# Kernel tuning notes

Hardware: AMD Instinct MI355X
Metric: run time of the kernel (lower is better)

The kernel has to match this reference:

```python
import jax, jax.numpy as jnp
import numpy as np

BN_EPS = 1e-5


def _bn(x, gamma, beta):
    # BatchNorm1d in training mode: batch mean, biased variance
    m = jnp.mean(x, axis=0)
    v = jnp.var(x, axis=0)
    return (x - m) * jax.lax.rsqrt(v + BN_EPS) * gamma + beta


def _gin_rel(h_src, h_dst, src, dst, W1, W2, g1, b1, g2, b2):
    # GINConv (eps=0): sum-aggregate src features onto dst, add self feature
    n_dst = h_dst.shape[0]
    agg = jax.ops.segment_sum(h_src[src], dst, num_segments=n_dst)  # [N_dst, d]
    x = h_dst + agg
    # MLP: Linear -> BN -> ReLU -> Linear  (both Linears bias=False)
    h = jax.nn.relu(_bn(x @ W1, g1, b1)) @ W2
    # GINBase: BN -> ReLU
    return jax.nn.relu(_bn(h, g2, b2))


def setup_inputs() -> dict:
    key = jax.random.key(0)
    ks = jax.random.split(key, 12)
    N_U, N_I, E, D = 50000, 50000, 640000, 128
    s = 1.0 / np.sqrt(D)
    inp = {
        "h_user": jax.random.normal(ks[0], (N_U, D), jnp.float32),
        "h_item": jax.random.normal(ks[1], (N_I, D), jnp.float32),
        "src_rates": jax.random.randint(ks[2], (E,), 0, N_U, jnp.int32),
        "dst_rates": jax.random.randint(ks[3], (E,), 0, N_I, jnp.int32),
        "src_rev": jax.random.randint(ks[4], (E,), 0, N_I, jnp.int32),
        "dst_rev": jax.random.randint(ks[5], (E,), 0, N_U, jnp.int32),
        "W1_rates": jax.random.normal(ks[6], (D, D), jnp.float32) * s,
        "W2_rates": jax.random.normal(ks[7], (D, D), jnp.float32) * s,
        "g1_rates": jnp.ones((D,), jnp.float32),
        "b1_rates": jnp.zeros((D,), jnp.float32),
        "g2_rates": jnp.ones((D,), jnp.float32),
        "b2_rates": jnp.zeros((D,), jnp.float32),
        "W1_rev": jax.random.normal(ks[8], (D, D), jnp.float32) * s,
        "W2_rev": jax.random.normal(ks[9], (D, D), jnp.float32) * s,
        "g1_rev": jnp.ones((D,), jnp.float32),
        "b1_rev": jnp.zeros((D,), jnp.float32),
        "g2_rev": jnp.ones((D,), jnp.float32),
        "b2_rev": jnp.zeros((D,), jnp.float32),
    }
    return inp


def reference(h_user, h_item, src_rates, dst_rates, src_rev, dst_rev,
              W1_rates, W2_rates, g1_rates, b1_rates, g2_rates, b2_rates,
              W1_rev, W2_rev, g1_rev, b1_rev, g2_rev, b2_rev):
    # relation 'rates': user -> item; relation 'rated_by': item -> user
    out_item = _gin_rel(h_user, h_item, src_rates, dst_rates,
                        W1_rates, W2_rates, g1_rates, b1_rates, g2_rates, b2_rates)
    out_user = _gin_rel(h_item, h_user, src_rev, dst_rev,
                        W1_rev, W2_rev, g1_rev, b1_rev, g2_rev, b2_rev)
    # HeteroGraphConv sums per dst type; one relation per dst type here.
    # GINLayer squeezes each output (no-op for 2D tensors).
    return (out_user, out_item)
```

## Files before the change

kernel.cpp:

```cpp
#include <hip/hip_runtime.h>

#define D 128
#define NBUK 8
#define NCH 32
#define BWMAX 8192
#define FILL_FINE 2048
static constexpr float BN_EPS = 1e-5f;

typedef __attribute__((ext_vector_type(8))) short short8;
typedef __attribute__((ext_vector_type(4))) float f32x4;

__device__ __forceinline__ unsigned short f2bf(float f)
{
    unsigned u = __builtin_bit_cast(unsigned, f);
    unsigned r = u + 0x7fffu + ((u >> 16) & 1u);
    return (unsigned short)(r >> 16);
}
__device__ __forceinline__ float bflo(unsigned u)
{
    return __builtin_bit_cast(float, u << 16);
}
__device__ __forceinline__ float bfhi(unsigned u)
{
    return __builtin_bit_cast(float, u & 0xffff0000u);
}

struct CsrRel {
    const int* src; const int* dst;
    int* counts; int* offsets; int* bsum; int* perm; int* rank; int* pc;
    int E; int N; int nscan;
};
struct GatherRel {
    const unsigned short* hb; const float* hdst;
    const int* offsets; const int* perm;
    unsigned short* x; int N;
};
struct GemmRel {
    const unsigned short* X; const unsigned short* Wt;
    const float* insum; const float* insq; const float* gg; const float* bb;
    unsigned short* Y; float* osum; float* osq;
    int N; int ntiles;
};
struct OutRel {
    const unsigned short* z;
    const float* sum; const float* sq; const float* gg; const float* bb;
    float* out; int N;
};

__global__ __launch_bounds__(256) void prep_kernel(
    const float* __restrict__ hu, const float* __restrict__ hi,
    unsigned short* __restrict__ bu, unsigned short* __restrict__ bi8,
    int nu8, int ni8,
    const float* __restrict__ Wa, const float* __restrict__ Wb,
    const float* __restrict__ Wc, const float* __restrict__ Wd,
    unsigned short* __restrict__ wt, float* __restrict__ stats)
{
    const int t = threadIdx.x;
    if (blockIdx.x < 64) {
        const int wsel = blockIdx.x >> 4;
        const float* W = wsel == 0 ? Wa : wsel == 1 ? Wb : wsel == 2 ? Wc : Wd;
        unsigned short* out = wt + (size_t)wsel * D * D;
        const int tile = blockIdx.x & 15;
        const int k0 = (tile >> 2) * 32, n0 = (tile & 3) * 32;
        __shared__ float s[32][33];
        const int r = t >> 3, c = (t & 7) * 4;
        float4 v = *reinterpret_cast<const float4*>(W + (size_t)(k0 + r) * D + n0 + c);
        s[r][c] = v.x; s[r][c + 1] = v.y; s[r][c + 2] = v.z; s[r][c + 3] = v.w;
        __syncthreads();
        unsigned lo = (unsigned)f2bf(s[c][r]) | ((unsigned)f2bf(s[c + 1][r]) << 16);
        unsigned hi = (unsigned)f2bf(s[c + 2][r]) | ((unsigned)f2bf(s[c + 3][r]) << 16);
        *reinterpret_cast<uint2*>(out + (size_t)(n0 + r) * D + k0 + c) =
            make_uint2(lo, hi);
        return;
    }
    if (blockIdx.x == 64) {
        reinterpret_cast<float4*>(stats)[t] = make_float4(0.f, 0.f, 0.f, 0.f);
        return;
    }
    int i = (blockIdx.x - 65) * 256 + t;
    if (i >= nu8 + ni8) return;
    const float* s; unsigned short* d; int o;
    if (i < nu8) { s = hu; d = bu; o = i; }
    else         { s = hi; d = bi8; o = i - nu8; }
    float4 v0 = reinterpret_cast<const float4*>(s)[o * 2];
    float4 v1 = reinterpret_cast<const float4*>(s)[o * 2 + 1];
    uint4 r;
    r.x = (unsigned)f2bf(v0.x) | ((unsigned)f2bf(v0.y) << 16);
    r.y = (unsigned)f2bf(v0.z) | ((unsigned)f2bf(v0.w) << 16);
    r.z = (unsigned)f2bf(v1.x) | ((unsigned)f2bf(v1.y) << 16);
    r.w = (unsigned)f2bf(v1.z) | ((unsigned)f2bf(v1.w) << 16);
    reinterpret_cast<uint4*>(d)[o] = r;
}

__global__ __launch_bounds__(256) void hist_kernel(CsrRel r0, CsrRel r1)
{
    CsrRel r = blockIdx.y ? r1 : r0;
    __shared__ int h[BWMAX];
    const int b = blockIdx.x & (NBUK - 1);
    const int c = blockIdx.x >> 3;
    const int bw = (r.N + NBUK - 1) / NBUK;
    const int lo = b * bw;
    const int hi = min(lo + bw, r.N);
    const int CE = (r.E + NCH - 1) / NCH;
    const int e1 = min(c * CE + CE, r.E);

    for (int j = threadIdx.x; j < bw; j += 256) h[j] = 0;
    __syncthreads();
    for (int e = c * CE + threadIdx.x; e < e1; e += 256) {
        int d = r.dst[e];
        if (d >= lo && d < hi)
            r.rank[e] = atomicAdd(&h[d - lo], 1);
    }
    __syncthreads();
    int* out = r.pc + (size_t)(b * NCH + c) * bw;
    for (int j = threadIdx.x; j < bw; j += 256) out[j] = h[j];
}

__global__ __launch_bounds__(256) void chunkpfx_kernel(CsrRel r0, CsrRel r1)
{
    CsrRel r = blockIdx.y ? r1 : r0;
    const int t = threadIdx.x;
    int d = blockIdx.x * 256 + t;
    int s = 0;
    if (d < r.N) {
        const int bw = (r.N + NBUK - 1) / NBUK;
        int b = d / bw, j = d - b * bw;
        int* base = r.pc + (size_t)b * NCH * bw + j;
        for (int c = 0; c < NCH; ++c) {
            int v = base[(size_t)c * bw];
            base[(size_t)c * bw] = s;
            s += v;
        }
        r.counts[d] = s;
    }
    __shared__ int red[256];
    red[t] = s;
    __syncthreads();
    for (int off = 128; off > 0; off >>= 1) {
        if (t < off) red[t] += red[t + off];
        __syncthreads();
    }
    if (t == 0) r.bsum[blockIdx.x] = red[0];
}

__global__ __launch_bounds__(256) void scan_partials_kernel(CsrRel rr0, CsrRel rr1)
{
    CsrRel r = blockIdx.y ? rr1 : rr0;
    __shared__ int part[256];
    const int t = threadIdx.x;
    int v = (t < r.nscan) ? r.bsum[t] : 0;
    part[t] = v;
    __syncthreads();
    for (int off = 1; off < 256; off <<= 1) {
        int tmp = (t >= off) ? part[t - off] : 0;
        __syncthreads();
        part[t] += tmp;
        __syncthreads();
    }
    if (t < r.nscan) r.bsum[t] = part[t] - v;
}

__global__ __launch_bounds__(256) void scan_block_kernel(CsrRel rr0, CsrRel rr1)
{
    CsrRel r = blockIdx.y ? rr1 : rr0;
    if ((int)blockIdx.x >= r.nscan) return;
    __shared__ int part[256];
    const int t = threadIdx.x;
    const int d = blockIdx.x * 256 + t;
    int v = (d < r.N) ? r.counts[d] : 0;
    part[t] = v;
    __syncthreads();
    for (int off = 1; off < 256; off <<= 1) {
        int tmp = (t >= off) ? part[t - off] : 0;
        __syncthreads();
        part[t] += tmp;
        __syncthreads();
    }
    int excl = part[t] - v + r.bsum[blockIdx.x];
    if (d < r.N) {
        r.offsets[d] = excl;
        if (d == r.N - 1) r.offsets[r.N] = excl + v;
    }
}

__global__ __launch_bounds__(256) void fill_kernel(CsrRel rr0, CsrRel rr1)
{
    CsrRel r = blockIdx.y ? rr1 : rr0;
    const int b = blockIdx.x & (NBUK - 1);
    const int fc = blockIdx.x >> 3;
    const int f0 = fc * FILL_FINE;
    if (f0 >= r.E) return;
    const int f1 = min(f0 + FILL_FINE, r.E);
    const int bw = (r.N + NBUK - 1) / NBUK;
    const int lo = b * bw;
    const int hi = min(lo + bw, r.N);
    const int CE = (r.E + NCH - 1) / NCH;
    const int c0 = f0 / CE;
    const int cb = (c0 + 1) * CE;
    const int* pcb0 = r.pc + (size_t)(b * NCH + c0) * bw;
    const int* pcb1 = pcb0 + bw;
    for (int e = f0 + threadIdx.x; e < f1; e += 256) {
        int d = r.dst[e];
        if (d >= lo && d < hi) {
            const int* pcb = (e >= cb) ? pcb1 : pcb0;
            r.perm[r.offsets[d] + pcb[d - lo] + r.rank[e]] = r.src[e];
        }
    }
}

__global__ __launch_bounds__(256) void gather_agg_kernel(GatherRel g0, GatherRel g1)
{
    GatherRel g = blockIdx.y ? g1 : g0;
    int row = blockIdx.x * 4 + (threadIdx.x >> 6);
    row = __builtin_amdgcn_readfirstlane(row);
    if (row >= g.N) return;
    const int c = (threadIdx.x & 63) * 2;
    const int beg = g.offsets[row], end = g.offsets[row + 1];
    float2 acc = *reinterpret_cast<const float2*>(g.hdst + (size_t)row * D + c);
    const unsigned short* hb = g.hb;
    int i = beg;
    for (; i + 7 < end; i += 8) {
        unsigned u[8];
#pragma unroll
        for (int k = 0; k < 8; ++k) {
            int s = g.perm[i + k];
            u[k] = *reinterpret_cast<const unsigned*>(hb + (size_t)s * D + c);
        }
        float ax = 0.f, ay = 0.f;
#pragma unroll
        for (int k = 0; k < 8; ++k) { ax += bflo(u[k]); ay += bfhi(u[k]); }
        acc.x += ax;
        acc.y += ay;
    }
    if (i + 3 < end) {
        int s0 = g.perm[i], s1 = g.perm[i + 1];
        int s2 = g.perm[i + 2], s3 = g.perm[i + 3];
        unsigned u0 = *reinterpret_cast<const unsigned*>(hb + (size_t)s0 * D + c);
        unsigned u1 = *reinterpret_cast<const unsigned*>(hb + (size_t)s1 * D + c);
        unsigned u2 = *reinterpret_cast<const unsigned*>(hb + (size_t)s2 * D + c);
        unsigned u3 = *reinterpret_cast<const unsigned*>(hb + (size_t)s3 * D + c);
        acc.x += (bflo(u0) + bflo(u1)) + (bflo(u2) + bflo(u3));
        acc.y += (bfhi(u0) + bfhi(u1)) + (bfhi(u2) + bfhi(u3));
        i += 4;
    }
    for (; i < end; ++i) {
        unsigned u = *reinterpret_cast<const unsigned*>(hb + (size_t)g.perm[i] * D + c);
        acc.x += bflo(u);
        acc.y += bfhi(u);
    }
    unsigned o = (unsigned)f2bf(acc.x) | ((unsigned)f2bf(acc.y) << 16);
    *reinterpret_cast<unsigned*>(g.x + (size_t)row * D + c) = o;
}

__device__ __forceinline__ unsigned bnpack(unsigned u, float sLo, float sHi,
                                           float bLo, float bHi)
{
    float lo = fmaxf(fmaf(bflo(u), sLo, bLo), 0.f);
    float hi = fmaxf(fmaf(bfhi(u), sHi, bHi), 0.f);
    return (unsigned)f2bf(lo) | ((unsigned)f2bf(hi) << 16);
}

template <bool BN_IN>
__global__ __launch_bounds__(256, 2) void gemm_stats_kernel(GemmRel q0, GemmRel q1)
{
    GemmRel q = blockIdx.y ? q1 : q0;
    const int t = threadIdx.x;
    const int w = t >> 6;
    const int l = t & 63;
    const int lr = l & 15;
    const int lk = (l >> 4) << 3;

    __shared__ float s_sc[D], s_bi[D];
    if constexpr (BN_IN) {
        if (t < D) {
            float inv_n = 1.f / (float)q.N;
            float mean = q.insum[t] * inv_n;
            float var = fmaxf(q.insq[t] * inv_n - mean * mean, 0.f);
            float s = q.gg[t] * rsqrtf(var + BN_EPS);
            s_sc[t] = s;
            s_bi[t] = q.bb[t] - mean * s;
        }
        __syncthreads();
    }

    uint4 wf[4][8];
#pragma unroll
    for (int kk = 0; kk < 4; ++kk)
#pragma unroll
        for (int n = 0; n < 8; ++n)
            wf[kk][n] = *reinterpret_cast<const uint4*>(
                q.Wt + (size_t)(n * 16 + lr) * D + kk * 32 + lk);

    float ps[8], pq[8];
#pragma unroll
    for (int n = 0; n < 8; ++n) { ps[n] = 0.f; pq[n] = 0.f; }

    for (int tile = blockIdx.x; tile < q.ntiles; tile += gridDim.x) {
        const int arow = tile * 64 + w * 16 + lr;
        f32x4 acc[8];
#pragma unroll
        for (int n = 0; n < 8; ++n) acc[n] = (f32x4){0.f, 0.f, 0.f, 0.f};

#pragma unroll
        for (int kk = 0; kk < 4; ++kk) {
            uint4 a4 = make_uint4(0u, 0u, 0u, 0u);
            if (arow < q.N) {
                a4 = *reinterpret_cast<const uint4*>(
                    q.X + (size_t)arow * D + kk * 32 + lk);
                if constexpr (BN_IN) {
                    const int kb = kk * 32 + lk;
                    float4 s0 = *reinterpret_cast<const float4*>(&s_sc[kb]);
                    float4 s1 = *reinterpret_cast<const float4*>(&s_sc[kb + 4]);
                    float4 b0 = *reinterpret_cast<const float4*>(&s_bi[kb]);
                    float4 b1 = *reinterpret_cast<const float4*>(&s_bi[kb + 4]);
                    a4.x = bnpack(a4.x, s0.x, s0.y, b0.x, b0.y);
                    a4.y = bnpack(a4.y, s0.z, s0.w, b0.z, b0.w);
                    a4.z = bnpack(a4.z, s1.x, s1.y, b1.x, b1.y);
                    a4.w = bnpack(a4.w, s1.z, s1.w, b1.z, b1.w);
                }
            }
            short8 a = __builtin_bit_cast(short8, a4);
#pragma unroll
            for (int n = 0; n < 8; ++n)
                acc[n] = __builtin_amdgcn_mfma_f32_16x16x32_bf16(
                    a, __builtin_bit_cast(short8, wf[kk][n]), acc[n], 0, 0, 0);
        }

        const int orow = tile * 64 + w * 16 + (l >> 4) * 4;
#pragma unroll
        for (int n = 0; n < 8; ++n) {
#pragma unroll
            for (int j = 0; j < 4; ++j) {
                float v = acc[n][j];
                ps[n] += v;
                pq[n] += v * v;
                if (orow + j < q.N)
                    q.Y[(size_t)(orow + j) * D + n * 16 + lr] = f2bf(v);
            }
        }
    }

#pragma unroll
    for (int n = 0; n < 8; ++n) {
        ps[n] += __shfl_xor(ps[n], 16); ps[n] += __shfl_xor(ps[n], 32);
        pq[n] += __shfl_xor(pq[n], 16); pq[n] += __shfl_xor(pq[n], 32);
    }
    __shared__ float ssum[4][D], ssq[4][D];
    if (l < 16) {
#pragma unroll
        for (int n = 0; n < 8; ++n) {
            ssum[w][n * 16 + l] = ps[n];
            ssq[w][n * 16 + l]  = pq[n];
        }
    }
    __syncthreads();
    if (t < D) {
        float a = ssum[0][t] + ssum[1][t] + ssum[2][t] + ssum[3][t];
        float b = ssq[0][t] + ssq[1][t] + ssq[2][t] + ssq[3][t];
        atomicAdd(&q.osum[t], a);
        atomicAdd(&q.osq[t], b);
    }
}

__global__ __launch_bounds__(256) void bn_relu_out_kernel(OutRel o0, OutRel o1)
{
    OutRel o = blockIdx.y ? o1 : o0;
    __shared__ float s_sc[D], s_bi[D];
    if (threadIdx.x < D) {
        int c = threadIdx.x;
        float inv_n = 1.f / (float)o.N;
        float mean = o.sum[c] * inv_n;
        float var = fmaxf(o.sq[c] * inv_n - mean * mean, 0.f);
        float s = o.gg[c] * rsqrtf(var + BN_EPS);
        s_sc[c] = s;
        s_bi[c] = o.bb[c] - mean * s;
    }
    __syncthreads();

    const int n8 = o.N * (D / 8);
    for (int i = blockIdx.x * blockDim.x + threadIdx.x; i < n8;
         i += gridDim.x * blockDim.x) {
        uint4 z = reinterpret_cast<const uint4*>(o.z)[i];
        int c = (i * 8) & (D - 1);
        float4 s0 = *reinterpret_cast<const float4*>(&s_sc[c]);
        float4 s1 = *reinterpret_cast<const float4*>(&s_sc[c + 4]);
        float4 b0 = *reinterpret_cast<const float4*>(&s_bi[c]);
        float4 b1 = *reinterpret_cast<const float4*>(&s_bi[c + 4]);
        float4 r0, r1;
        r0.x = fmaxf(fmaf(bflo(z.x), s0.x, b0.x), 0.f);
        r0.y = fmaxf(fmaf(bfhi(z.x), s0.y, b0.y), 0.f);
        r0.z = fmaxf(fmaf(bflo(z.y), s0.z, b0.z), 0.f);
        r0.w = fmaxf(fmaf(bfhi(z.y), s0.w, b0.w), 0.f);
        r1.x = fmaxf(fmaf(bflo(z.z), s1.x, b1.x), 0.f);
        r1.y = fmaxf(fmaf(bfhi(z.z), s1.y, b1.y), 0.f);
        r1.z = fmaxf(fmaf(bflo(z.w), s1.z, b1.z), 0.f);
        r1.w = fmaxf(fmaf(bfhi(z.w), s1.w, b1.w), 0.f);
        reinterpret_cast<float4*>(o.out)[i * 2] = r0;
        reinterpret_cast<float4*>(o.out)[i * 2 + 1] = r1;
    }
}

extern "C" void kernel_launch(void* const* d_in, const int* in_sizes, int n_in,
                              void* d_out, int out_size, void* d_ws, size_t ws_size,
                              hipStream_t stream)
{
    const float* h_user   = (const float*)d_in[0];
    const float* h_item   = (const float*)d_in[1];
    const int* src_rates  = (const int*)d_in[2];
    const int* dst_rates  = (const int*)d_in[3];
    const int* src_rev    = (const int*)d_in[4];
    const int* dst_rev    = (const int*)d_in[5];
    const float* W1_rates = (const float*)d_in[6];
    const float* W2_rates = (const float*)d_in[7];
    const float* g1_rates = (const float*)d_in[8];
    const float* b1_rates = (const float*)d_in[9];
    const float* g2_rates = (const float*)d_in[10];
    const float* b2_rates = (const float*)d_in[11];
    const float* W1_rev   = (const float*)d_in[12];
    const float* W2_rev   = (const float*)d_in[13];
    const float* g1_rev   = (const float*)d_in[14];
    const float* b1_rev   = (const float*)d_in[15];
    const float* g2_rev   = (const float*)d_in[16];
    const float* b2_rev   = (const float*)d_in[17];

    const int n_user = in_sizes[0] / D;
    const int n_item = in_sizes[1] / D;
    const int E1 = in_sizes[2];
    const int E2 = in_sizes[4];

    const int bw0 = (n_item + NBUK - 1) / NBUK;
    const int bw1 = (n_user + NBUK - 1) / NBUK;

    char* p = (char*)d_ws;
    auto alloc = [&](size_t bytes) {
        char* q = p;
        p += (bytes + 255) & ~(size_t)255;
        return q;
    };
    unsigned short* hbu = (unsigned short*)alloc((size_t)n_user * D * 2);
    unsigned short* hbi = (unsigned short*)alloc((size_t)n_item * D * 2);
    unsigned short* xz0 = (unsigned short*)alloc((size_t)n_item * D * 2);
    unsigned short* xz1 = (unsigned short*)alloc((size_t)n_user * D * 2);
    unsigned short* yb0 = (unsigned short*)alloc((size_t)n_item * D * 2);
    unsigned short* yb1 = (unsigned short*)alloc((size_t)n_user * D * 2);
    unsigned short* wt  = (unsigned short*)alloc((size_t)4 * D * D * 2);
    float* stats   = (float*)alloc((size_t)8 * D * 4);
    int* counts0   = (int*)alloc((size_t)n_item * 4);
    int* counts1   = (int*)alloc((size_t)n_user * 4);
    int* offsets0  = (int*)alloc(((size_t)n_item + 1) * 4);
    int* offsets1  = (int*)alloc(((size_t)n_user + 1) * 4);
    int* bsum0     = (int*)alloc((size_t)256 * 4);
    int* bsum1     = (int*)alloc((size_t)256 * 4);
    int* perm0     = (int*)alloc((size_t)E1 * 4);
    int* perm1     = (int*)alloc((size_t)E2 * 4);
    int* rank0     = (int*)alloc((size_t)E1 * 4);
    int* rank1     = (int*)alloc((size_t)E2 * 4);
    int* pc0       = (int*)alloc((size_t)NBUK * NCH * bw0 * 4);
    int* pc1       = (int*)alloc((size_t)NBUK * NCH * bw1 * 4);

    float* out_user = (float*)d_out;
    float* out_item = out_user + (size_t)n_user * D;

    const int nu8 = n_user * D / 8, ni8 = n_item * D / 8;
    int pblocks = 65 + (nu8 + ni8 + 255) / 256;
    prep_kernel<<<pblocks, 256, 0, stream>>>(
        h_user, h_item, hbu, hbi, nu8, ni8,
        W1_rates, W2_rates, W1_rev, W2_rev, wt, stats);

    float* st0 = stats;
    float* st1 = stats + 4 * D;

    CsrRel c0 = {src_rates, dst_rates, counts0, offsets0, bsum0, perm0, rank0,
                 pc0, E1, n_item, (n_item + 255) / 256};
    CsrRel c1 = {src_rev, dst_rev, counts1, offsets1, bsum1, perm1, rank1,
                 pc1, E2, n_user, (n_user + 255) / 256};

    int ns = c0.nscan > c1.nscan ? c0.nscan : c1.nscan;
    int nmax = n_item > n_user ? n_item : n_user;
    int emax = E1 > E2 ? E1 : E2;
    hist_kernel<<<dim3(NBUK * NCH, 2), 256, 0, stream>>>(c0, c1);
    chunkpfx_kernel<<<dim3(ns, 2), 256, 0, stream>>>(c0, c1);
    scan_partials_kernel<<<dim3(1, 2), 256, 0, stream>>>(c0, c1);
    scan_block_kernel<<<dim3(ns, 2), 256, 0, stream>>>(c0, c1);
    int nfine = (emax + FILL_FINE - 1) / FILL_FINE;
    fill_kernel<<<dim3(NBUK * nfine, 2), 256, 0, stream>>>(c0, c1);

    GatherRel ga0 = {hbu, h_item, offsets0, perm0, xz0, n_item};
    GatherRel ga1 = {hbi, h_user, offsets1, perm1, xz1, n_user};
    int ab = (nmax + 3) / 4;
    gather_agg_kernel<<<dim3(ab, 2), 256, 0, stream>>>(ga0, ga1);

    const int nt0 = (n_item + 63) / 64, nt1 = (n_user + 63) / 64;
    int gx = nt0 > nt1 ? nt0 : nt1;
    if (gx > 256) gx = 256;

    GemmRel q10 = {xz0, wt,             nullptr, nullptr, nullptr, nullptr,
                   yb0, st0, st0 + D, n_item, nt0};
    GemmRel q11 = {xz1, wt + 2 * D * D, nullptr, nullptr, nullptr, nullptr,
                   yb1, st1, st1 + D, n_user, nt1};
    gemm_stats_kernel<false><<<dim3(gx, 2), 256, 0, stream>>>(q10, q11);

    GemmRel q20 = {yb0, wt + D * D,     st0, st0 + D, g1_rates, b1_rates,
                   xz0, st0 + 2 * D, st0 + 3 * D, n_item, nt0};
    GemmRel q21 = {yb1, wt + 3 * D * D, st1, st1 + D, g1_rev, b1_rev,
                   xz1, st1 + 2 * D, st1 + 3 * D, n_user, nt1};
    gemm_stats_kernel<true><<<dim3(gx, 2), 256, 0, stream>>>(q20, q21);

    OutRel o0 = {xz0, st0 + 2 * D, st0 + 3 * D, g2_rates, b2_rates,
                 out_item, n_item};
    OutRel o1 = {xz1, st1 + 2 * D, st1 + 3 * D, g2_rev, b2_rev,
                 out_user, n_user};
    int n8m = nmax * (D / 8);
    int ob = (n8m + 255) / 256;
    if (ob > 2048) ob = 2048;
    bn_relu_out_kernel<<<dim3(ob, 2), 256, 0, stream>>>(o0, o1);
}
```

Before: 206.3 us.

## Pack CSR histogram counters into 16-bit pairs to cover all destinations per block

```diff
diff --git a/kernel.cpp b/kernel.cpp
--- a/kernel.cpp
+++ b/kernel.cpp
@@ -2,9 +2,8 @@
 
 #define D 128
 #define NBUK 8
-#define NCH 32
-#define BWMAX 8192
-#define FILL_FINE 2048
+#define NCHF 128
+#define LDSW 32768
 static constexpr float BN_EPS = 1e-5f;
 
 typedef __attribute__((ext_vector_type(8))) short short8;
@@ -27,7 +26,8 @@
 
 struct CsrRel {
     const int* src; const int* dst;
-    int* counts; int* offsets; int* bsum; int* perm; int* rank; int* pc;
+    int* counts; int* offsets; int* bsum; int* perm;
+    unsigned short* rank16; unsigned* pc;
     int E; int N; int nscan;
 };
 struct GatherRel {
@@ -95,43 +95,61 @@
 __global__ __launch_bounds__(256) void hist_kernel(CsrRel r0, CsrRel r1)
 {
     CsrRel r = blockIdx.y ? r1 : r0;
-    __shared__ int h[BWMAX];
-    const int b = blockIdx.x & (NBUK - 1);
-    const int c = blockIdx.x >> 3;
-    const int bw = (r.N + NBUK - 1) / NBUK;
-    const int lo = b * bw;
-    const int hi = min(lo + bw, r.N);
-    const int CE = (r.E + NCH - 1) / NCH;
-    const int e1 = min(c * CE + CE, r.E);
-
-    for (int j = threadIdx.x; j < bw; j += 256) h[j] = 0;
-    __syncthreads();
-    for (int e = c * CE + threadIdx.x; e < e1; e += 256) {
+    __shared__ unsigned h2[LDSW];
+    const int t = threadIdx.x;
+    const int c = blockIdx.x;
+    const int CE = (r.E + NCHF - 1) / NCHF;
+    const int e0 = c * CE;
+    const int e1 = min(e0 + CE, r.E);
+    const int bw2 = (r.N + 1) >> 1;
+
+    const int bw4 = bw2 & ~3;
+    for (int i = t * 4; i < bw4; i += 1024)
+        *reinterpret_cast<uint4*>(&h2[i]) = make_uint4(0u, 0u, 0u, 0u);
+    for (int i = bw4 + t; i < bw2; i += 256) h2[i] = 0u;
+    __syncthreads();
+
+    for (int e = e0 + t; e < e1; e += 256) {
         int d = r.dst[e];
-        if (d >= lo && d < hi)
-            r.rank[e] = atomicAdd(&h[d - lo], 1);
-    }
-    __syncthreads();
-    int* out = r.pc + (size_t)(b * NCH + c) * bw;
-    for (int j = threadIdx.x; j < bw; j += 256) out[j] = h[j];
+        unsigned sh = (unsigned)(d & 1) * 16u;
+        unsigned old = atomicAdd(&h2[d >> 1], 1u << sh);
+        r.rank16[e] = (unsigned short)((old >> sh) & 0xffffu);
+    }
+    __syncthreads();
+
+    unsigned* out = r.pc + (size_t)c * bw2;
+    for (int i = t * 4; i < bw4; i += 1024)
+        *reinterpret_cast<uint4*>(&out[i]) = *reinterpret_cast<uint4*>(&h2[i]);
+    for (int i = bw4 + t; i < bw2; i += 256) out[i] = h2[i];
 }
 
 __global__ __launch_bounds__(256) void chunkpfx_kernel(CsrRel r0, CsrRel r1)
 {
     CsrRel r = blockIdx.y ? r1 : r0;
+    __shared__ unsigned lds[NCHF * 256];
     const int t = threadIdx.x;
-    int d = blockIdx.x * 256 + t;
+    const int j = blockIdx.x * 256 + t;
+    const int bw2 = (r.N + 1) >> 1;
     int s = 0;
-    if (d < r.N) {
-        const int bw = (r.N + NBUK - 1) / NBUK;
-        int b = d / bw, j = d - b * bw;
-        int* base = r.pc + (size_t)b * NCH * bw + j;
-        for (int c = 0; c < NCH; ++c) {
-            int v = base[(size_t)c * bw];
-            base[(size_t)c * bw] = s;
-            s += v;
-        }
-        r.counts[d] = s;
+    if (j < bw2) {
+        const unsigned* base = r.pc + j;
+#pragma unroll 4
+        for (int c = 0; c < NCHF; ++c)
+            lds[c * 256 + t] = base[(size_t)c * bw2];
+        unsigned s0 = 0, s1 = 0;
+        for (int c = 0; c < NCHF; ++c) {
+            unsigned v = lds[c * 256 + t];
+            lds[c * 256 + t] = s0 | (s1 << 16);
+            s0 += v & 0xffffu;
+            s1 += v >> 16;
+        }
+        unsigned* wb = r.pc + j;
+#pragma unroll 4
+        for (int c = 0; c < NCHF; ++c)
+            wb[(size_t)c * bw2] = lds[c * 256 + t];
+        r.counts[2 * j] = (int)s0;
+        if (2 * j + 1 < r.N) r.counts[2 * j + 1] = (int)s1; else s1 = 0;
+        s = (int)(s0 + s1);
     }
     __shared__ int red[256];
     red[t] = s;
@@ -166,9 +184,11 @@
     if ((int)blockIdx.x >= r.nscan) return;
     __shared__ int part[256];
     const int t = threadIdx.x;
-    const int d = blockIdx.x * 256 + t;
-    int v = (d < r.N) ? r.counts[d] : 0;
-    part[t] = v;
+    const int j = blockIdx.x * 256 + t;
+    int v0 = (2 * j < r.N) ? r.counts[2 * j] : 0;
+    int v1 = (2 * j + 1 < r.N) ? r.counts[2 * j + 1] : 0;
+    int s = v0 + v1;
+    part[t] = s;
     __syncthreads();
     for (int off = 1; off < 256; off <<= 1) {
         int tmp = (t >= off) ? part[t - off] : 0;
@@ -176,34 +196,32 @@
         part[t] += tmp;
         __syncthreads();
     }
-    int excl = part[t] - v + r.bsum[blockIdx.x];
-    if (d < r.N) {
-        r.offsets[d] = excl;
-        if (d == r.N - 1) r.offsets[r.N] = excl + v;
-    }
+    int excl = part[t] - s + r.bsum[blockIdx.x];
+    if (2 * j < r.N) r.offsets[2 * j] = excl;
+    if (2 * j + 1 < r.N) r.offsets[2 * j + 1] = excl + v0;
+    if (2 * j == r.N - 1 || 2 * j + 1 == r.N - 1) r.offsets[r.N] = excl + s;
 }
 
 __global__ __launch_bounds__(256) void fill_kernel(CsrRel rr0, CsrRel rr1)
 {
     CsrRel r = blockIdx.y ? rr1 : rr0;
     const int b = blockIdx.x & (NBUK - 1);
-    const int fc = blockIdx.x >> 3;
-    const int f0 = fc * FILL_FINE;
-    if (f0 >= r.E) return;
-    const int f1 = min(f0 + FILL_FINE, r.E);
+    const int c = blockIdx.x >> 3;
+    const int CE = (r.E + NCHF - 1) / NCHF;
+    const int e0 = c * CE;
+    if (e0 >= r.E) return;
+    const int e1 = min(e0 + CE, r.E);
     const int bw = (r.N + NBUK - 1) / NBUK;
     const int lo = b * bw;
     const int hi = min(lo + bw, r.N);
-    const int CE = (r.E + NCH - 1) / NCH;
-    const int c0 = f0 / CE;
-    const int cb = (c0 + 1) * CE;
-    const int* pcb0 = r.pc + (size_t)(b * NCH + c0) * bw;
-    const int* pcb1 = pcb0 + bw;
-    for (int e = f0 + threadIdx.x; e < f1; e += 256) {
+    const int bw2 = (r.N + 1) >> 1;
+    const unsigned* pcc = r.pc + (size_t)c * bw2;
+    for (int e = e0 + threadIdx.x; e < e1; e += 256) {
         int d = r.dst[e];
         if (d >= lo && d < hi) {
-            const int* pcb = (e >= cb) ? pcb1 : pcb0;
-            r.perm[r.offsets[d] + pcb[d - lo] + r.rank[e]] = r.src[e];
+            unsigned sh = (unsigned)(d & 1) * 16u;
+            int px = (int)((pcc[d >> 1] >> sh) & 0xffffu);
+            r.perm[r.offsets[d] + px + (int)r.rank16[e]] = r.src[e];
         }
     }
 }
@@ -428,8 +446,8 @@
     const int E1 = in_sizes[2];
     const int E2 = in_sizes[4];
 
-    const int bw0 = (n_item + NBUK - 1) / NBUK;
-    const int bw1 = (n_user + NBUK - 1) / NBUK;
+    const int bw2_0 = (n_item + 1) >> 1;
+    const int bw2_1 = (n_user + 1) >> 1;
 
     char* p = (char*)d_ws;
     auto alloc = [&](size_t bytes) {
@@ -453,10 +471,10 @@
     int* bsum1     = (int*)alloc((size_t)256 * 4);
     int* perm0     = (int*)alloc((size_t)E1 * 4);
     int* perm1     = (int*)alloc((size_t)E2 * 4);
-    int* rank0     = (int*)alloc((size_t)E1 * 4);
-    int* rank1     = (int*)alloc((size_t)E2 * 4);
-    int* pc0       = (int*)alloc((size_t)NBUK * NCH * bw0 * 4);
-    int* pc1       = (int*)alloc((size_t)NBUK * NCH * bw1 * 4);
+    unsigned short* rank0 = (unsigned short*)alloc((size_t)E1 * 2);
+    unsigned short* rank1 = (unsigned short*)alloc((size_t)E2 * 2);
+    unsigned* pc0  = (unsigned*)alloc((size_t)NCHF * bw2_0 * 4);
+    unsigned* pc1  = (unsigned*)alloc((size_t)NCHF * bw2_1 * 4);
 
     float* out_user = (float*)d_out;
     float* out_item = out_user + (size_t)n_user * D;
@@ -470,20 +488,18 @@
     float* st0 = stats;
     float* st1 = stats + 4 * D;
 
-    CsrRel c0 = {src_rates, dst_rates, counts0, offsets0, bsum0, perm0, rank0,
-                 pc0, E1, n_item, (n_item + 255) / 256};
-    CsrRel c1 = {src_rev, dst_rev, counts1, offsets1, bsum1, perm1, rank1,
-                 pc1, E2, n_user, (n_user + 255) / 256};
+    CsrRel c0 = {src_rates, dst_rates, counts0, offsets0, bsum0, perm0,
+                 rank0, pc0, E1, n_item, (n_item + 511) / 512};
+    CsrRel c1 = {src_rev, dst_rev, counts1, offsets1, bsum1, perm1,
+                 rank1, pc1, E2, n_user, (n_user + 511) / 512};
 
     int ns = c0.nscan > c1.nscan ? c0.nscan : c1.nscan;
     int nmax = n_item > n_user ? n_item : n_user;
-    int emax = E1 > E2 ? E1 : E2;
-    hist_kernel<<<dim3(NBUK * NCH, 2), 256, 0, stream>>>(c0, c1);
+    hist_kernel<<<dim3(NCHF, 2), 256, 0, stream>>>(c0, c1);
     chunkpfx_kernel<<<dim3(ns, 2), 256, 0, stream>>>(c0, c1);
     scan_partials_kernel<<<dim3(1, 2), 256, 0, stream>>>(c0, c1);
     scan_block_kernel<<<dim3(ns, 2), 256, 0, stream>>>(c0, c1);
-    int nfine = (emax + FILL_FINE - 1) / FILL_FINE;
-    fill_kernel<<<dim3(NBUK * nfine, 2), 256, 0, stream>>>(c0, c1);
+    fill_kernel<<<dim3(NBUK * NCHF, 2), 256, 0, stream>>>(c0, c1);
 
     GatherRel ga0 = {hbu, h_item, offsets0, perm0, xz0, n_item};
     GatherRel ga1 = {hbi, h_user, offsets1, perm1, xz1, n_user};
```

Result: no change. 203.6 us (-1.3%).
